# Optimization experiments

Measured on AMD Instinct MI355X. Metric: run time of the kernel, lower is better.

Reference implementation:

```python
import jax, jax.numpy as jnp
import numpy as np

N_NODES = 100_000
N_EDGES = 1_600_000
N_GRAPHS = 64
IN_CH = 128
HID = 64
OUT_CH = 2


def setup_inputs() -> dict:
    key = jax.random.key(0)
    ks = jax.random.split(key, 12)

    def lin(k, fan_in, fan_out):
        s = 1.0 / np.sqrt(fan_in)
        return jax.random.uniform(k, (fan_in, fan_out), jnp.float32, -s, s)

    x = jax.random.normal(ks[0], (N_NODES, IN_CH), jnp.float32)
    edge_index = jax.random.randint(ks[1], (2, N_EDGES), 0, N_NODES, jnp.int64)
    batch = jnp.sort(jax.random.randint(ks[2], (N_NODES,), 0, N_GRAPHS, jnp.int64))
    return {
        "x": x,
        "edge_index": edge_index,
        "batch": batch,
        "w_rel0": lin(ks[3], IN_CH, HID),
        "b_rel0": jnp.zeros((HID,), jnp.float32),
        "w_root0": lin(ks[4], IN_CH, HID),
        "w_rel1": lin(ks[5], HID, HID),
        "b_rel1": jnp.zeros((HID,), jnp.float32),
        "w_root1": lin(ks[6], HID, HID),
        "w_rel2": lin(ks[7], HID, HID),
        "b_rel2": jnp.zeros((HID,), jnp.float32),
        "w_root2": lin(ks[8], HID, HID),
        "head_w1": lin(ks[9], HID, HID),
        "head_b1": jnp.zeros((HID,), jnp.float32),
        "head_w2": lin(ks[10], HID, OUT_CH),
        "head_b2": jnp.zeros((OUT_CH,), jnp.float32),
    }


def _graph_conv(x, src, dst, w_rel, b_rel, w_root):
    # PyG GraphConv: out = lin_rel(sum_{j->i} x_j) + lin_root(x_i)
    agg = jax.ops.segment_sum(x[src], dst, num_segments=N_NODES)  # [N, d_in]
    return agg @ w_rel + b_rel + x @ w_root


def reference(x, edge_index, batch, w_rel0, b_rel0, w_root0,
              w_rel1, b_rel1, w_root1, w_rel2, b_rel2, w_root2,
              head_w1, head_b1, head_w2, head_b2):
    src, dst = edge_index[0], edge_index[1]
    h = jax.nn.relu(_graph_conv(x, src, dst, w_rel0, b_rel0, w_root0))
    h = jax.nn.relu(_graph_conv(h, src, dst, w_rel1, b_rel1, w_root1))
    h = jax.nn.relu(_graph_conv(h, src, dst, w_rel2, b_rel2, w_root2))
    # global_mean_pool over graph ids (dropout is identity at inference)
    sums = jax.ops.segment_sum(h, batch, num_segments=N_GRAPHS)          # [G, H]
    cnts = jax.ops.segment_sum(jnp.ones((N_NODES,), h.dtype), batch,
                               num_segments=N_GRAPHS)                    # [G]
    pooled = sums / jnp.maximum(cnts, 1.0)[:, None]
    z = jax.nn.relu(pooled @ head_w1 + head_b1)
    return z @ head_w2 + head_b2
```

## Files before the change

### kernel.cpp

```cpp
#include <hip/hip_runtime.h>
#include <hip/hip_bf16.h>

#define CAP 64
#define KBUCK 391
#define BSHIFT 8
#define BCAP 4608
#define CHUNK_A 2048

typedef __attribute__((ext_vector_type(8))) short short8;
typedef __attribute__((ext_vector_type(4))) float f32x4;

__device__ inline unsigned short bfbits(float f) {
    __hip_bfloat16 b = __float2bfloat16(f);
    unsigned short u;
    __builtin_memcpy(&u, &b, 2);
    return u;
}

__global__ __launch_bounds__(256) void bucket_edges_kernel(
    const int* __restrict__ ei, int E, int* __restrict__ gcur, int2* __restrict__ bucketed)
{
    __shared__ int hist[KBUCK];
    __shared__ int base[KBUCK];
    const int e0 = blockIdx.x * CHUNK_A;
    const int e1 = min(e0 + CHUNK_A, E);
    for (int i = threadIdx.x; i < KBUCK; i += 256) hist[i] = 0;
    __syncthreads();
    for (int e = e0 + threadIdx.x; e < e1; e += 256)
        atomicAdd(&hist[ei[E + e] >> BSHIFT], 1);
    __syncthreads();
    for (int i = threadIdx.x; i < KBUCK; i += 256) {
        int h = hist[i];
        base[i] = h ? atomicAdd(&gcur[i], h) : 0;
        hist[i] = 0;
    }
    __syncthreads();
    for (int e = e0 + threadIdx.x; e < e1; e += 256) {
        int s = ei[e], d = ei[E + e];
        int b = d >> BSHIFT;
        int off = base[b] + atomicAdd(&hist[b], 1);
        if (off < BCAP) bucketed[(size_t)b * BCAP + off] = make_int2(s, d);
    }
}

__global__ __launch_bounds__(256) void build_slots_kernel(
    const int2* __restrict__ bucketed, const int* __restrict__ gcur,
    int* __restrict__ cnt, int* __restrict__ slots, int N)
{
    __shared__ int lcnt[256];
    const int b = blockIdx.x;
    const int nb0 = b << BSHIFT;
    lcnt[threadIdx.x] = 0;
    __syncthreads();
    const int count = min(gcur[b], BCAP);
    const int2* src = bucketed + (size_t)b * BCAP;
    for (int i = threadIdx.x; i < count; i += 256) {
        int2 sd = src[i];
        int pos = atomicAdd(&lcnt[sd.y - nb0], 1);
        if (pos < CAP) slots[(size_t)sd.y * CAP + pos] = sd.x;
    }
    __syncthreads();
    int node = nb0 + threadIdx.x;
    if (node < N) cnt[node] = min(lcnt[threadIdx.x], CAP);
}

__global__ __launch_bounds__(256) void prep_weights_kernel(
    const float* __restrict__ wr0, const float* __restrict__ wt0,
    const float* __restrict__ wr1, const float* __restrict__ wt1,
    const float* __restrict__ wr2, const float* __restrict__ wt2,
    __hip_bfloat16* __restrict__ hi, __hip_bfloat16* __restrict__ lo)
{
    int idx = blockIdx.x * 256 + threadIdx.x;
    if (idx >= 32768) return;
    const float *wr, *wt;
    int n, k;
    if (idx < 16384)      { wr = wr0; wt = wt0; int r = idx;         n = r >> 7; k = r & 127; }
    else if (idx < 24576) { wr = wr1; wt = wt1; int r = idx - 16384; n = r >> 6; k = r & 63; }
    else                  { wr = wr2; wt = wt2; int r = idx - 24576; n = r >> 6; k = r & 63; }
    float w = (n < 64) ? wr[k * 64 + n] : wt[k * 64 + (n - 64)];
    __hip_bfloat16 h = __float2bfloat16(w);
    hi[idx] = h;
    lo[idx] = __float2bfloat16(w - __bfloat162float(h));
}

template <int DIN, bool AFP32>
__global__ __launch_bounds__(256) void mfma_lin_kernel(
    const void* __restrict__ featv,
    const __hip_bfloat16* __restrict__ whiT, const __hip_bfloat16* __restrict__ wloT,
    const float* __restrict__ b_rel,
    __hip_bfloat16* __restrict__ y, float* __restrict__ r, int N)
{
    __shared__ __hip_bfloat16 As[128][48];
    __shared__ __hip_bfloat16 Bh[128][48];
    __shared__ __hip_bfloat16 Bl[128][48];
    const int t = threadIdx.x;
    const int lane = t & 63;
    const int wid = t >> 6;
    const int wm = wid >> 1, wn = wid & 1;
    const int node0 = blockIdx.x * 128;
    const int lrow = lane & 15;
    const int kgrp = lane >> 4;

    f32x4 acc[4][4];
    #pragma unroll
    for (int i = 0; i < 4; ++i)
        #pragma unroll
        for (int j = 0; j < 4; ++j) acc[i][j] = (f32x4){0.f, 0.f, 0.f, 0.f};

    for (int ks = 0; ks < DIN / 32; ++ks) {
        #pragma unroll
        for (int p = 0; p < 2; ++p) {
            int c = t + p * 256;
            int m = c >> 2, kc = c & 3;
            int row = node0 + m; if (row >= N) row = N - 1;
            if (AFP32) {
                const float* feat = (const float*)featv;
                const float* src = feat + (size_t)row * DIN + ks * 32 + kc * 8;
                float4 v0 = *(const float4*)src;
                float4 v1 = *(const float4*)(src + 4);
                union { uint4 q; unsigned short s[8]; } pk;
                pk.s[0] = bfbits(v0.x); pk.s[1] = bfbits(v0.y);
                pk.s[2] = bfbits(v0.z); pk.s[3] = bfbits(v0.w);
                pk.s[4] = bfbits(v1.x); pk.s[5] = bfbits(v1.y);
                pk.s[6] = bfbits(v1.z); pk.s[7] = bfbits(v1.w);
                *(uint4*)&As[m][kc * 8] = pk.q;
            } else {
                const __hip_bfloat16* feat = (const __hip_bfloat16*)featv;
                *(uint4*)&As[m][kc * 8] =
                    *(const uint4*)(feat + (size_t)row * DIN + ks * 32 + kc * 8);
            }
        }
        #pragma unroll
        for (int p = 0; p < 4; ++p) {
            int c = t + p * 256;
            int half = c >> 9;
            int cc = c & 511;
            int n = cc >> 2, kc = cc & 3;
            const __hip_bfloat16* w = half ? wloT : whiT;
            uint4 v = *(const uint4*)(w + (size_t)n * DIN + ks * 32 + kc * 8);
            if (half) *(uint4*)&Bl[n][kc * 8] = v;
            else      *(uint4*)&Bh[n][kc * 8] = v;
        }
        __syncthreads();

        short8 a[4], bh[4], bl[4];
        #pragma unroll
        for (int i = 0; i < 4; ++i)
            a[i] = *(const short8*)&As[wm * 64 + i * 16 + lrow][kgrp * 8];
        #pragma unroll
        for (int j = 0; j < 4; ++j) {
            bh[j] = *(const short8*)&Bh[wn * 64 + j * 16 + lrow][kgrp * 8];
            bl[j] = *(const short8*)&Bl[wn * 64 + j * 16 + lrow][kgrp * 8];
        }
        #pragma unroll
        for (int i = 0; i < 4; ++i)
            #pragma unroll
            for (int j = 0; j < 4; ++j) {
                acc[i][j] = __builtin_amdgcn_mfma_f32_16x16x32_bf16(a[i], bh[j], acc[i][j], 0, 0, 0);
                acc[i][j] = __builtin_amdgcn_mfma_f32_16x16x32_bf16(a[i], bl[j], acc[i][j], 0, 0, 0);
            }
        __syncthreads();
    }

    #pragma unroll
    for (int i = 0; i < 4; ++i) {
        int mbase = node0 + wm * 64 + i * 16 + kgrp * 4;
        #pragma unroll
        for (int j = 0; j < 4; ++j) {
            int n = wn * 64 + j * 16 + lrow;
            #pragma unroll
            for (int v = 0; v < 4; ++v) {
                int m = mbase + v;
                if (m < N) {
                    float val = acc[i][j][v];
                    if (n < 64) y[(size_t)m * 64 + n] = __float2bfloat16(val);
                    else        r[(size_t)m * 64 + (n - 64)] = val + b_rel[n - 64];
                }
            }
        }
    }
}

__global__ __launch_bounds__(256) void gather_relu_kernel(
    const __hip_bfloat16* __restrict__ y, const int* __restrict__ cnt,
    const int* __restrict__ slots, const float* __restrict__ rin,
    __hip_bfloat16* __restrict__ hout, int N)
{
    const int node = blockIdx.x * 8 + (threadIdx.x >> 5);
    if (node >= N) return;
    const int sub = threadIdx.x & 31;
    const int nb = sub >> 3;
    const int ch = (sub & 7) * 8;
    const int deg = cnt[node];
    const int* sl = slots + (size_t)node * CAP;
    const unsigned short* yp = (const unsigned short*)y;

    float a[8], b[8];
    #pragma unroll
    for (int k = 0; k < 8; ++k) { a[k] = 0.f; b[k] = 0.f; }

    #pragma unroll 2
    for (int j = nb; j < deg; j += 8) {
        int n0 = sl[j];
        uint4 v = *(const uint4*)(yp + (size_t)n0 * 64 + ch);
        a[0] += __uint_as_float(v.x << 16); a[1] += __uint_as_float(v.x & 0xffff0000u);
        a[2] += __uint_as_float(v.y << 16); a[3] += __uint_as_float(v.y & 0xffff0000u);
        a[4] += __uint_as_float(v.z << 16); a[5] += __uint_as_float(v.z & 0xffff0000u);
        a[6] += __uint_as_float(v.w << 16); a[7] += __uint_as_float(v.w & 0xffff0000u);
        int j2 = j + 4;
        if (j2 < deg) {
            int n1 = sl[j2];
            uint4 w = *(const uint4*)(yp + (size_t)n1 * 64 + ch);
            b[0] += __uint_as_float(w.x << 16); b[1] += __uint_as_float(w.x & 0xffff0000u);
            b[2] += __uint_as_float(w.y << 16); b[3] += __uint_as_float(w.y & 0xffff0000u);
            b[4] += __uint_as_float(w.z << 16); b[5] += __uint_as_float(w.z & 0xffff0000u);
            b[6] += __uint_as_float(w.w << 16); b[7] += __uint_as_float(w.w & 0xffff0000u);
        }
    }
    #pragma unroll
    for (int k = 0; k < 8; ++k) {
        a[k] += b[k];
        a[k] += __shfl_xor(a[k], 8);
        a[k] += __shfl_xor(a[k], 16);
    }
    if (nb == 0) {
        float4 r0 = *(const float4*)&rin[(size_t)node * 64 + ch];
        float4 r1 = *(const float4*)&rin[(size_t)node * 64 + ch + 4];
        float f0 = fmaxf(r0.x + a[0], 0.f), f1 = fmaxf(r0.y + a[1], 0.f);
        float f2 = fmaxf(r0.z + a[2], 0.f), f3 = fmaxf(r0.w + a[3], 0.f);
        float f4 = fmaxf(r1.x + a[4], 0.f), f5 = fmaxf(r1.y + a[5], 0.f);
        float f6 = fmaxf(r1.z + a[6], 0.f), f7 = fmaxf(r1.w + a[7], 0.f);
        union { uint4 q; unsigned short s[8]; } pk;
        pk.s[0] = bfbits(f0); pk.s[1] = bfbits(f1); pk.s[2] = bfbits(f2); pk.s[3] = bfbits(f3);
        pk.s[4] = bfbits(f4); pk.s[5] = bfbits(f5); pk.s[6] = bfbits(f6); pk.s[7] = bfbits(f7);
        *(uint4*)((unsigned short*)hout + (size_t)node * 64 + ch) = pk.q;
    }
}

__global__ __launch_bounds__(256) void pool_kernel(
    const __hip_bfloat16* __restrict__ h, const int* __restrict__ batch,
    float* __restrict__ gsum, int* __restrict__ gcnt, int N)
{
    const int CHUNK = 64;
    int wid = (blockIdx.x * 256 + threadIdx.x) >> 6;
    int lane = threadIdx.x & 63;
    int nb = lane >> 3;
    int ch = (lane & 7) * 8;
    int start = wid * CHUNK;
    if (start >= N) return;
    int end = min(start + CHUNK, N);
    const unsigned short* hp = (const unsigned short*)h;

    float a[8];
    #pragma unroll
    for (int k = 0; k < 8; ++k) a[k] = 0.f;
    int runcnt = 0;
    int i = start;
    int gcur = batch[start];

    while (i < end) {
        int idx = i + lane; if (idx > end - 1) idx = end - 1;
        int bl = batch[idx];
        unsigned long long diff = __ballot(bl != gcur && (i + lane) < end);
        int len = diff ? ((int)__ffsll(diff) - 1) : min(64, end - i);
        for (int j = i + nb; j < i + len; j += 8) {
            uint4 v = *(const uint4*)(hp + (size_t)j * 64 + ch);
            a[0] += __uint_as_float(v.x << 16); a[1] += __uint_as_float(v.x & 0xffff0000u);
            a[2] += __uint_as_float(v.y << 16); a[3] += __uint_as_float(v.y & 0xffff0000u);
            a[4] += __uint_as_float(v.z << 16); a[5] += __uint_as_float(v.z & 0xffff0000u);
            a[6] += __uint_as_float(v.w << 16); a[7] += __uint_as_float(v.w & 0xffff0000u);
        }
        runcnt += len;
        i += len;
        if (diff) {
            #pragma unroll
            for (int k = 0; k < 8; ++k) {
                a[k] += __shfl_xor(a[k], 8);
                a[k] += __shfl_xor(a[k], 16);
                a[k] += __shfl_xor(a[k], 32);
            }
            if (runcnt > 0) {
                if (nb == 0) {
                    #pragma unroll
                    for (int k = 0; k < 8; ++k)
                        atomicAdd(&gsum[gcur * 64 + ch + k], a[k]);
                }
                if (lane == 0) atomicAdd(&gcnt[gcur], runcnt);
            }
            #pragma unroll
            for (int k = 0; k < 8; ++k) a[k] = 0.f;
            runcnt = 0;
            gcur = __shfl(bl, len);
        }
    }
    #pragma unroll
    for (int k = 0; k < 8; ++k) {
        a[k] += __shfl_xor(a[k], 8);
        a[k] += __shfl_xor(a[k], 16);
        a[k] += __shfl_xor(a[k], 32);
    }
    if (runcnt > 0) {
        if (nb == 0) {
            #pragma unroll
            for (int k = 0; k < 8; ++k)
                atomicAdd(&gsum[gcur * 64 + ch + k], a[k]);
        }
        if (lane == 0) atomicAdd(&gcnt[gcur], runcnt);
    }
}

__global__ __launch_bounds__(256) void head_kernel(
    const float* __restrict__ gsum, const int* __restrict__ gcnt,
    const float* __restrict__ w1, const float* __restrict__ b1,
    const float* __restrict__ w2, const float* __restrict__ b2,
    float* __restrict__ out)
{
    __shared__ float pm[64 * 64];
    __shared__ float z[64 * 64];
    int t = threadIdx.x;
    for (int i = t; i < 64 * 64; i += 256) {
        int g = i >> 6;
        float cf = (float)gcnt[g];
        if (cf < 1.f) cf = 1.f;
        pm[i] = gsum[i] / cf;
    }
    __syncthreads();
    for (int i = t; i < 64 * 64; i += 256) {
        int g = i >> 6, c = i & 63;
        float a = b1[c];
        #pragma unroll 8
        for (int k = 0; k < 64; ++k) a = fmaf(pm[g * 64 + k], w1[k * 64 + c], a);
        z[i] = fmaxf(a, 0.f);
    }
    __syncthreads();
    for (int i = t; i < 64 * 2; i += 256) {
        int g = i >> 1, o = i & 1;
        float a = b2[o];
        #pragma unroll 8
        for (int k = 0; k < 64; ++k) a = fmaf(z[g * 64 + k], w2[k * 2 + o], a);
        out[i] = a;
    }
}

extern "C" void kernel_launch(void* const* d_in, const int* in_sizes, int n_in,
                              void* d_out, int out_size, void* d_ws, size_t ws_size,
                              hipStream_t stream)
{
    const float* x       = (const float*)d_in[0];
    const int*   ei      = (const int*)d_in[1];
    const int*   batch   = (const int*)d_in[2];
    const float* w_rel0  = (const float*)d_in[3];
    const float* b_rel0  = (const float*)d_in[4];
    const float* w_root0 = (const float*)d_in[5];
    const float* w_rel1  = (const float*)d_in[6];
    const float* b_rel1  = (const float*)d_in[7];
    const float* w_root1 = (const float*)d_in[8];
    const float* w_rel2  = (const float*)d_in[9];
    const float* b_rel2  = (const float*)d_in[10];
    const float* w_root2 = (const float*)d_in[11];
    const float* hw1     = (const float*)d_in[12];
    const float* hb1     = (const float*)d_in[13];
    const float* hw2     = (const float*)d_in[14];
    const float* hb2     = (const float*)d_in[15];
    float* out = (float*)d_out;

    const int N = in_sizes[0] / 128;
    const int E = in_sizes[1] / 2;
    const int G = 64;

    size_t off = 0;
    auto alloc = [&](size_t bytes) -> void* {
        void* p = (char*)d_ws + off;
        off += (bytes + 255) & ~(size_t)255;
        return p;
    };
    int*   cnt      = (int*)alloc((size_t)N * 4);
    int*   slots    = (int*)alloc((size_t)N * CAP * 4);
    int2*  bucketed = (int2*)alloc((size_t)KBUCK * BCAP * 8);
    int*   gcur     = (int*)alloc((size_t)KBUCK * 4);
    __hip_bfloat16* whiT = (__hip_bfloat16*)alloc(32768 * 2);
    __hip_bfloat16* wloT = (__hip_bfloat16*)alloc(32768 * 2);
    __hip_bfloat16* ybf  = (__hip_bfloat16*)alloc((size_t)N * 64 * 2);
    __hip_bfloat16* h0   = (__hip_bfloat16*)alloc((size_t)N * 64 * 2);
    __hip_bfloat16* h1   = (__hip_bfloat16*)alloc((size_t)N * 64 * 2);
    float* rbuf     = (float*)alloc((size_t)N * 64 * 4);
    float* gsum     = (float*)alloc((size_t)G * 64 * 4);
    int*   gcnt     = (int*)alloc((size_t)G * 4);
    (void)ws_size; (void)n_in;

    hipMemsetAsync(gcur, 0, (size_t)KBUCK * 4, stream);
    hipMemsetAsync(gsum, 0, (size_t)G * 64 * 4, stream);
    hipMemsetAsync(gcnt, 0, (size_t)G * 4, stream);

    prep_weights_kernel<<<128, 256, 0, stream>>>(w_rel0, w_root0, w_rel1, w_root1,
                                                 w_rel2, w_root2, whiT, wloT);
    bucket_edges_kernel<<<(E + CHUNK_A - 1) / CHUNK_A, 256, 0, stream>>>(ei, E, gcur, bucketed);
    build_slots_kernel<<<KBUCK, 256, 0, stream>>>(bucketed, gcur, cnt, slots, N);

    const int gemm_blocks = (N + 127) / 128;
    const int gather_blocks = (N + 7) / 8;
    mfma_lin_kernel<128, true><<<gemm_blocks, 256, 0, stream>>>(
        x, whiT, wloT, b_rel0, ybf, rbuf, N);
    gather_relu_kernel<<<gather_blocks, 256, 0, stream>>>(ybf, cnt, slots, rbuf, h0, N);

    mfma_lin_kernel<64, false><<<gemm_blocks, 256, 0, stream>>>(
        h0, whiT + 16384, wloT + 16384, b_rel1, ybf, rbuf, N);
    gather_relu_kernel<<<gather_blocks, 256, 0, stream>>>(ybf, cnt, slots, rbuf, h1, N);

    mfma_lin_kernel<64, false><<<gemm_blocks, 256, 0, stream>>>(
        h1, whiT + 24576, wloT + 24576, b_rel2, ybf, rbuf, N);
    gather_relu_kernel<<<gather_blocks, 256, 0, stream>>>(ybf, cnt, slots, rbuf, h0, N);

    int pool_waves  = (N + 63) / 64;
    int pool_blocks = (pool_waves + 3) / 4;
    pool_kernel<<<pool_blocks, 256, 0, stream>>>(h0, batch, gsum, gcnt, N);
    head_kernel<<<1, 256, 0, stream>>>(gsum, gcnt, hw1, hb1, hw2, hb2, out);
}
```

Baseline: 385.4 us.

## Fuse layer-0 GEMM with edge bucketing, pack bucket entries, store root term in bf16

The layer-0 MFMA GEMM and the edge-bucketing pass now run in one launch, with block index deciding which body a block runs, so the two independent stages overlap and one launch is saved. Bucketed edges are packed into a single 32-bit word (source shifted left by 8, low 8 bits of destination), which halves the intermediate traffic. The destination index is kept in registers between the histogram and scatter passes so it is not re-read. The root/bias term is stored as bf16 instead of fp32, halving its write and read bandwidth at some cost in precision. The packing assumes source ids fit in 24 bits.

```diff
diff --git a/kernel.cpp b/kernel.cpp
--- a/kernel.cpp
+++ b/kernel.cpp
@@ -6,6 +6,8 @@
 #define BSHIFT 8
 #define BCAP 4608
 #define CHUNK_A 2048
+#define AITER (CHUNK_A / 256)
+#define LDSZ 36864
 
 typedef __attribute__((ext_vector_type(8))) short short8;
 typedef __attribute__((ext_vector_type(4))) float f32x4;
@@ -17,17 +19,23 @@
     return u;
 }
 
-__global__ __launch_bounds__(256) void bucket_edges_kernel(
-    const int* __restrict__ ei, int E, int* __restrict__ gcur, int2* __restrict__ bucketed)
-{
-    __shared__ int hist[KBUCK];
-    __shared__ int base[KBUCK];
-    const int e0 = blockIdx.x * CHUNK_A;
+__device__ inline void bucket_body(char* smem, int bb, const int* __restrict__ ei,
+                                   int E, int* __restrict__ gcur,
+                                   unsigned* __restrict__ bucketed)
+{
+    int* hist = (int*)smem;
+    int* base = hist + KBUCK;
+    const int e0 = bb * CHUNK_A;
     const int e1 = min(e0 + CHUNK_A, E);
     for (int i = threadIdx.x; i < KBUCK; i += 256) hist[i] = 0;
     __syncthreads();
-    for (int e = e0 + threadIdx.x; e < e1; e += 256)
-        atomicAdd(&hist[ei[E + e] >> BSHIFT], 1);
+    int dreg[AITER];
+    #pragma unroll
+    for (int it = 0; it < AITER; ++it) {
+        int e = e0 + it * 256 + threadIdx.x;
+        dreg[it] = (e < e1) ? ei[E + e] : -1;
+        if (dreg[it] >= 0) atomicAdd(&hist[dreg[it] >> BSHIFT], 1);
+    }
     __syncthreads();
     for (int i = threadIdx.x; i < KBUCK; i += 256) {
         int h = hist[i];
@@ -35,16 +43,22 @@
         hist[i] = 0;
     }
     __syncthreads();
-    for (int e = e0 + threadIdx.x; e < e1; e += 256) {
-        int s = ei[e], d = ei[E + e];
-        int b = d >> BSHIFT;
-        int off = base[b] + atomicAdd(&hist[b], 1);
-        if (off < BCAP) bucketed[(size_t)b * BCAP + off] = make_int2(s, d);
+    #pragma unroll
+    for (int it = 0; it < AITER; ++it) {
+        int e = e0 + it * 256 + threadIdx.x;
+        if (e < e1) {
+            int s = ei[e];
+            int d = dreg[it];
+            int b = d >> BSHIFT;
+            int off = base[b] + atomicAdd(&hist[b], 1);
+            if (off < BCAP)
+                bucketed[(size_t)b * BCAP + off] = ((unsigned)s << 8) | (unsigned)(d & 255);
+        }
     }
 }
 
 __global__ __launch_bounds__(256) void build_slots_kernel(
-    const int2* __restrict__ bucketed, const int* __restrict__ gcur,
+    const unsigned* __restrict__ bucketed, const int* __restrict__ gcur,
     int* __restrict__ cnt, int* __restrict__ slots, int N)
 {
     __shared__ int lcnt[256];
@@ -53,11 +67,12 @@
     lcnt[threadIdx.x] = 0;
     __syncthreads();
     const int count = min(gcur[b], BCAP);
-    const int2* src = bucketed + (size_t)b * BCAP;
+    const unsigned* src = bucketed + (size_t)b * BCAP;
     for (int i = threadIdx.x; i < count; i += 256) {
-        int2 sd = src[i];
-        int pos = atomicAdd(&lcnt[sd.y - nb0], 1);
-        if (pos < CAP) slots[(size_t)sd.y * CAP + pos] = sd.x;
+        unsigned p = src[i];
+        int dl = (int)(p & 255u);
+        int pos = atomicAdd(&lcnt[dl], 1);
+        if (pos < CAP) slots[(size_t)(nb0 + dl) * CAP + pos] = (int)(p >> 8);
     }
     __syncthreads();
     int node = nb0 + threadIdx.x;
@@ -84,20 +99,20 @@
 }
 
 template <int DIN, bool AFP32>
-__global__ __launch_bounds__(256) void mfma_lin_kernel(
-    const void* __restrict__ featv,
+__device__ inline void mfma_body(
+    char* smem, int bx, const void* __restrict__ featv,
     const __hip_bfloat16* __restrict__ whiT, const __hip_bfloat16* __restrict__ wloT,
     const float* __restrict__ b_rel,
-    __hip_bfloat16* __restrict__ y, float* __restrict__ r, int N)
-{
-    __shared__ __hip_bfloat16 As[128][48];
-    __shared__ __hip_bfloat16 Bh[128][48];
-    __shared__ __hip_bfloat16 Bl[128][48];
+    __hip_bfloat16* __restrict__ y, __hip_bfloat16* __restrict__ r, int N)
+{
+    __hip_bfloat16* As = (__hip_bfloat16*)smem;
+    __hip_bfloat16* Bh = As + 128 * 48;
+    __hip_bfloat16* Bl = Bh + 128 * 48;
     const int t = threadIdx.x;
     const int lane = t & 63;
     const int wid = t >> 6;
     const int wm = wid >> 1, wn = wid & 1;
-    const int node0 = blockIdx.x * 128;
+    const int node0 = bx * 128;
     const int lrow = lane & 15;
     const int kgrp = lane >> 4;
 
@@ -123,10 +138,10 @@
                 pk.s[2] = bfbits(v0.z); pk.s[3] = bfbits(v0.w);
                 pk.s[4] = bfbits(v1.x); pk.s[5] = bfbits(v1.y);
                 pk.s[6] = bfbits(v1.z); pk.s[7] = bfbits(v1.w);
-                *(uint4*)&As[m][kc * 8] = pk.q;
+                *(uint4*)&As[m * 48 + kc * 8] = pk.q;
             } else {
                 const __hip_bfloat16* feat = (const __hip_bfloat16*)featv;
-                *(uint4*)&As[m][kc * 8] =
+                *(uint4*)&As[m * 48 + kc * 8] =
                     *(const uint4*)(feat + (size_t)row * DIN + ks * 32 + kc * 8);
             }
         }
@@ -138,19 +153,19 @@
             int n = cc >> 2, kc = cc & 3;
             const __hip_bfloat16* w = half ? wloT : whiT;
             uint4 v = *(const uint4*)(w + (size_t)n * DIN + ks * 32 + kc * 8);
-            if (half) *(uint4*)&Bl[n][kc * 8] = v;
-            else      *(uint4*)&Bh[n][kc * 8] = v;
+            if (half) *(uint4*)&Bl[n * 48 + kc * 8] = v;
+            else      *(uint4*)&Bh[n * 48 + kc * 8] = v;
         }
         __syncthreads();
 
         short8 a[4], bh[4], bl[4];
         #pragma unroll
         for (int i = 0; i < 4; ++i)
-            a[i] = *(const short8*)&As[wm * 64 + i * 16 + lrow][kgrp * 8];
+            a[i] = *(const short8*)&As[(wm * 64 + i * 16 + lrow) * 48 + kgrp * 8];
         #pragma unroll
         for (int j = 0; j < 4; ++j) {
-            bh[j] = *(const short8*)&Bh[wn * 64 + j * 16 + lrow][kgrp * 8];
-            bl[j] = *(const short8*)&Bl[wn * 64 + j * 16 + lrow][kgrp * 8];
+            bh[j] = *(const short8*)&Bh[(wn * 64 + j * 16 + lrow) * 48 + kgrp * 8];
+            bl[j] = *(const short8*)&Bl[(wn * 64 + j * 16 + lrow) * 48 + kgrp * 8];
         }
         #pragma unroll
         for (int i = 0; i < 4; ++i)
@@ -174,16 +189,42 @@
                 if (m < N) {
                     float val = acc[i][j][v];
                     if (n < 64) y[(size_t)m * 64 + n] = __float2bfloat16(val);
-                    else        r[(size_t)m * 64 + (n - 64)] = val + b_rel[n - 64];
+                    else        r[(size_t)m * 64 + (n - 64)] = __float2bfloat16(val + b_rel[n - 64]);
                 }
             }
         }
     }
 }
 
+__global__ __launch_bounds__(256) void fused_l0_kernel(
+    const float* __restrict__ x,
+    const __hip_bfloat16* __restrict__ whiT, const __hip_bfloat16* __restrict__ wloT,
+    const float* __restrict__ b_rel,
+    __hip_bfloat16* __restrict__ y, __hip_bfloat16* __restrict__ r, int N,
+    int gemm_blocks, const int* __restrict__ ei, int E,
+    int* __restrict__ gcur, unsigned* __restrict__ bucketed)
+{
+    extern __shared__ char smem[];
+    if ((int)blockIdx.x < gemm_blocks)
+        mfma_body<128, true>(smem, blockIdx.x, x, whiT, wloT, b_rel, y, r, N);
+    else
+        bucket_body(smem, blockIdx.x - gemm_blocks, ei, E, gcur, bucketed);
+}
+
+template <int DIN>
+__global__ __launch_bounds__(256) void mfma_lin_kernel(
+    const __hip_bfloat16* __restrict__ feat,
+    const __hip_bfloat16* __restrict__ whiT, const __hip_bfloat16* __restrict__ wloT,
+    const float* __restrict__ b_rel,
+    __hip_bfloat16* __restrict__ y, __hip_bfloat16* __restrict__ r, int N)
+{
+    extern __shared__ char smem[];
+    mfma_body<DIN, false>(smem, blockIdx.x, feat, whiT, wloT, b_rel, y, r, N);
+}
+
 __global__ __launch_bounds__(256) void gather_relu_kernel(
     const __hip_bfloat16* __restrict__ y, const int* __restrict__ cnt,
-    const int* __restrict__ slots, const float* __restrict__ rin,
+    const int* __restrict__ slots, const __hip_bfloat16* __restrict__ rin,
     __hip_bfloat16* __restrict__ hout, int N)
 {
     const int node = blockIdx.x * 8 + (threadIdx.x >> 5);
@@ -224,12 +265,15 @@
         a[k] += __shfl_xor(a[k], 16);
     }
     if (nb == 0) {
-        float4 r0 = *(const float4*)&rin[(size_t)node * 64 + ch];
-        float4 r1 = *(const float4*)&rin[(size_t)node * 64 + ch + 4];
-        float f0 = fmaxf(r0.x + a[0], 0.f), f1 = fmaxf(r0.y + a[1], 0.f);
-        float f2 = fmaxf(r0.z + a[2], 0.f), f3 = fmaxf(r0.w + a[3], 0.f);
-        float f4 = fmaxf(r1.x + a[4], 0.f), f5 = fmaxf(r1.y + a[5], 0.f);
-        float f6 = fmaxf(r1.z + a[6], 0.f), f7 = fmaxf(r1.w + a[7], 0.f);
+        uint4 rv = *(const uint4*)((const unsigned short*)rin + (size_t)node * 64 + ch);
+        float r0 = __uint_as_float(rv.x << 16), r1 = __uint_as_float(rv.x & 0xffff0000u);
+        float r2 = __uint_as_float(rv.y << 16), r3 = __uint_as_float(rv.y & 0xffff0000u);
+        float r4 = __uint_as_float(rv.z << 16), r5 = __uint_as_float(rv.z & 0xffff0000u);
+        float r6 = __uint_as_float(rv.w << 16), r7 = __uint_as_float(rv.w & 0xffff0000u);
+        float f0 = fmaxf(r0 + a[0], 0.f), f1 = fmaxf(r1 + a[1], 0.f);
+        float f2 = fmaxf(r2 + a[2], 0.f), f3 = fmaxf(r3 + a[3], 0.f);
+        float f4 = fmaxf(r4 + a[4], 0.f), f5 = fmaxf(r5 + a[5], 0.f);
+        float f6 = fmaxf(r6 + a[6], 0.f), f7 = fmaxf(r7 + a[7], 0.f);
         union { uint4 q; unsigned short s[8]; } pk;
         pk.s[0] = bfbits(f0); pk.s[1] = bfbits(f1); pk.s[2] = bfbits(f2); pk.s[3] = bfbits(f3);
         pk.s[4] = bfbits(f4); pk.s[5] = bfbits(f5); pk.s[6] = bfbits(f6); pk.s[7] = bfbits(f7);
@@ -374,16 +418,16 @@
         off += (bytes + 255) & ~(size_t)255;
         return p;
     };
-    int*   cnt      = (int*)alloc((size_t)N * 4);
-    int*   slots    = (int*)alloc((size_t)N * CAP * 4);
-    int2*  bucketed = (int2*)alloc((size_t)KBUCK * BCAP * 8);
-    int*   gcur     = (int*)alloc((size_t)KBUCK * 4);
+    int*      cnt      = (int*)alloc((size_t)N * 4);
+    int*      slots    = (int*)alloc((size_t)N * CAP * 4);
+    unsigned* bucketed = (unsigned*)alloc((size_t)KBUCK * BCAP * 4);
+    int*      gcur     = (int*)alloc((size_t)KBUCK * 4);
     __hip_bfloat16* whiT = (__hip_bfloat16*)alloc(32768 * 2);
     __hip_bfloat16* wloT = (__hip_bfloat16*)alloc(32768 * 2);
     __hip_bfloat16* ybf  = (__hip_bfloat16*)alloc((size_t)N * 64 * 2);
     __hip_bfloat16* h0   = (__hip_bfloat16*)alloc((size_t)N * 64 * 2);
     __hip_bfloat16* h1   = (__hip_bfloat16*)alloc((size_t)N * 64 * 2);
-    float* rbuf     = (float*)alloc((size_t)N * 64 * 4);
+    __hip_bfloat16* rbf  = (__hip_bfloat16*)alloc((size_t)N * 64 * 2);
     float* gsum     = (float*)alloc((size_t)G * 64 * 4);
     int*   gcnt     = (int*)alloc((size_t)G * 4);
     (void)ws_size; (void)n_in;
@@ -394,22 +438,23 @@
 
     prep_weights_kernel<<<128, 256, 0, stream>>>(w_rel0, w_root0, w_rel1, w_root1,
                                                  w_rel2, w_root2, whiT, wloT);
-    bucket_edges_kernel<<<(E + CHUNK_A - 1) / CHUNK_A, 256, 0, stream>>>(ei, E, gcur, bucketed);
+
+    const int gemm_blocks = (N + 127) / 128;
+    const int bucket_blocks = (E + CHUNK_A - 1) / CHUNK_A;
+    const int gather_blocks = (N + 7) / 8;
+
+    fused_l0_kernel<<<gemm_blocks + bucket_blocks, 256, LDSZ, stream>>>(
+        x, whiT, wloT, b_rel0, ybf, rbf, N, gemm_blocks, ei, E, gcur, bucketed);
     build_slots_kernel<<<KBUCK, 256, 0, stream>>>(bucketed, gcur, cnt, slots, N);
-
-    const int gemm_blocks = (N + 127) / 128;
-    const int gather_blocks = (N + 7) / 8;
-    mfma_lin_kernel<128, true><<<gemm_blocks, 256, 0, stream>>>(
-        x, whiT, wloT, b_rel0, ybf, rbuf, N);
-    gather_relu_kernel<<<gather_blocks, 256, 0, stream>>>(ybf, cnt, slots, rbuf, h0, N);
-
-    mfma_lin_kernel<64, false><<<gemm_blocks, 256, 0, stream>>>(
-        h0, whiT + 16384, wloT + 16384, b_rel1, ybf, rbuf, N);
-    gather_relu_kernel<<<gather_blocks, 256, 0, stream>>>(ybf, cnt, slots, rbuf, h1, N);
-
-    mfma_lin_kernel<64, false><<<gemm_blocks, 256, 0, stream>>>(
-        h1, whiT + 24576, wloT + 24576, b_rel2, ybf, rbuf, N);
-    gather_relu_kernel<<<gather_blocks, 256, 0, stream>>>(ybf, cnt, slots, rbuf, h0, N);
+    gather_relu_kernel<<<gather_blocks, 256, 0, stream>>>(ybf, cnt, slots, rbf, h0, N);
+
+    mfma_lin_kernel<64><<<gemm_blocks, 256, LDSZ, stream>>>(
+        h0, whiT + 16384, wloT + 16384, b_rel1, ybf, rbf, N);
+    gather_relu_kernel<<<gather_blocks, 256, 0, stream>>>(ybf, cnt, slots, rbf, h1, N);
+
+    mfma_lin_kernel<64><<<gemm_blocks, 256, LDSZ, stream>>>(
+        h1, whiT + 24576, wloT + 24576, b_rel2, ybf, rbf, N);
+    gather_relu_kernel<<<gather_blocks, 256, 0, stream>>>(ybf, cnt, slots, rbf, h0, N);
 
     int pool_waves  = (N + 63) / 64;
     int pool_blocks = (pool_waves + 3) / 4;
```

Result: faster. 376.0 us (-2.4%).
